# Kernel optimization log

Measured on AMD Instinct MI355X. Metric: run time of the kernel, lower is better.

## Reference

```python
import jax, jax.numpy as jnp
import numpy as np

N_NODES = 50000
N_EDGES = 300000
HIDDEN = 256


def setup_inputs() -> dict:
    key = jax.random.key(0)
    k_e, k_ei, k_rev, k_w, k_b = jax.random.split(key, 5)
    E = jax.random.normal(k_e, (N_EDGES, HIDDEN), dtype=jnp.float32)
    edge_index = jax.random.randint(k_ei, (2, N_EDGES), 0, N_NODES, dtype=jnp.int64)
    rev_index = jax.random.randint(k_rev, (N_EDGES,), 0, N_EDGES, dtype=jnp.int64)
    # Linear(hidden, hidden) params, torch-style: y = x @ W.T + b
    W = jax.random.normal(k_w, (HIDDEN, HIDDEN), dtype=jnp.float32) * (1.0 / np.sqrt(HIDDEN))
    b = jax.random.normal(k_b, (HIDDEN,), dtype=jnp.float32) * 0.01
    return {"E": E, "edge_index": edge_index, "rev_index": rev_index, "W": W, "b": b}


def reference(E, edge_index, rev_index, W, b):
    src, dest = edge_index[0], edge_index[1]
    H_uv = jax.nn.relu(E)                                   # [n_edges, hidden]
    # scatter-reduce (sum) edge messages into destination nodes
    M_v = jax.ops.segment_sum(H_uv, dest, num_segments=N_NODES)  # [n_nodes, hidden]
    # gather back to edges, subtract reverse-edge message
    M_uv = M_v[src] - H_uv[rev_index]                       # [n_edges, hidden]
    # linear update (dropout p=0 is identity)
    return M_uv @ W.T + b                                   # [n_edges, hidden]
```

## Files before the change

kernel.cpp:

```cpp
#include <hip/hip_runtime.h>
#include <hip/hip_bf16.h>

typedef unsigned short ushort_t;
typedef __attribute__((ext_vector_type(8))) short short8;
typedef __attribute__((ext_vector_type(4))) float f32x4;

#define HIDDEN 256
#define N_NODES 50000
#define BM 64
#define LDSROW 512

__device__ __forceinline__ unsigned int f2bf(float f) {
    union { float f; unsigned int i; } v; v.f = f;
    return (v.i + 0x7fffu + ((v.i >> 16) & 1u)) >> 16;
}
__device__ __forceinline__ float bf2f(unsigned int u) {
    union { unsigned int i; float f; } v; v.i = u << 16; return v.f;
}

#define OFF_MVB    0u
#define OFF_WF     25600000u
#define OFF_CNT    25731072u
#define OFF_OFFS   25931072u
#define OFF_CUR    26131076u
#define OFF_ELIST  26331076u
#define OFF_BSUM   27531076u

#define SCAN_NBLK ((N_NODES + 255) / 256)

__global__ void convert_w_frag(const float* __restrict__ W, ushort_t* __restrict__ Wf, int n) {
    int i = blockIdx.x * blockDim.x + threadIdx.x;
    if (i >= n) return;
    const int t    = i & 7;
    const int lane = (i >> 3) & 63;
    const int kk   = (i >> 9) & 7;
    const int g    = i >> 12;
    const int j = g * 16 + (lane & 15);
    const int k = kk * 32 + ((lane >> 4) & 3) * 8 + t;
    Wf[i] = (ushort_t)f2bf(W[j * HIDDEN + k]);
}

__global__ void count_dst(const int* __restrict__ dst, int* __restrict__ cnt, int n) {
    int i = blockIdx.x * blockDim.x + threadIdx.x;
    if (i < n) atomicAdd(&cnt[dst[i]], 1);
}

__global__ __launch_bounds__(256)
void block_scan(const int* __restrict__ cnt, int* __restrict__ offs,
                int* __restrict__ bsum) {
    __shared__ int sh[256];
    const int t = threadIdx.x;
    const int idx = blockIdx.x * 256 + t;
    int v = (idx < N_NODES) ? cnt[idx] : 0;
    sh[t] = v;
    __syncthreads();
    for (int off = 1; off < 256; off <<= 1) {
        int x = (t >= off) ? sh[t - off] : 0;
        __syncthreads();
        sh[t] += x;
        __syncthreads();
    }
    if (idx < N_NODES) offs[idx] = sh[t] - v;
    if (t == 255) bsum[blockIdx.x] = sh[255];
}

__global__ __launch_bounds__(256)
void scan_bsum(int* __restrict__ bsum, int nb) {
    __shared__ int sh[256];
    const int t = threadIdx.x;
    int v = (t < nb) ? bsum[t] : 0;
    sh[t] = v;
    __syncthreads();
    for (int off = 1; off < 256; off <<= 1) {
        int x = (t >= off) ? sh[t - off] : 0;
        __syncthreads();
        sh[t] += x;
        __syncthreads();
    }
    if (t < nb) bsum[t] = sh[t] - v;
}

__global__ __launch_bounds__(256)
void add_base(int* __restrict__ offs, const int* __restrict__ bsum,
              int* __restrict__ cur, int n_edges) {
    const int idx = blockIdx.x * 256 + threadIdx.x;
    if (idx < N_NODES) {
        int o = offs[idx] + bsum[idx >> 8];
        offs[idx] = o;
        cur[idx] = o;
    }
    if (idx == 0) offs[N_NODES] = n_edges;
}

__global__ void fill_elist(const int* __restrict__ dst, int* __restrict__ cur,
                           int* __restrict__ elist, int n) {
    int i = blockIdx.x * blockDim.x + threadIdx.x;
    if (i < n) {
        int d = dst[i];
        int pos = atomicAdd(&cur[d], 1);
        elist[pos] = i;
    }
}

__global__ __launch_bounds__(256)
void node_gather_sum(const float* __restrict__ E,
                     const int* __restrict__ offs,
                     const int* __restrict__ elist,
                     unsigned int* __restrict__ Mvb) {
    const int w    = blockIdx.x * 4 + (threadIdx.x >> 6);
    const int node = w >> 1;
    const int half = w & 1;
    const int lane = threadIdx.x & 63;
    if (node >= N_NODES) return;
    const float* Eh = E + half * 128 + lane * 2;
    const int s0 = offs[node];
    const int s1 = offs[node + 1];
    float ax = 0.f, ay = 0.f;
    int j = s0;
    for (; j + 4 <= s1; j += 4) {
        const int e0 = elist[j], e1 = elist[j + 1], e2 = elist[j + 2], e3 = elist[j + 3];
        float2 v0 = *(const float2*)(Eh + (size_t)e0 * HIDDEN);
        float2 v1 = *(const float2*)(Eh + (size_t)e1 * HIDDEN);
        float2 v2 = *(const float2*)(Eh + (size_t)e2 * HIDDEN);
        float2 v3 = *(const float2*)(Eh + (size_t)e3 * HIDDEN);
        ax += fmaxf(v0.x, 0.f) + fmaxf(v1.x, 0.f) + fmaxf(v2.x, 0.f) + fmaxf(v3.x, 0.f);
        ay += fmaxf(v0.y, 0.f) + fmaxf(v1.y, 0.f) + fmaxf(v2.y, 0.f) + fmaxf(v3.y, 0.f);
    }
    for (; j < s1; ++j) {
        float2 v = *(const float2*)(Eh + (size_t)elist[j] * HIDDEN);
        ax += fmaxf(v.x, 0.f);
        ay += fmaxf(v.y, 0.f);
    }
    Mvb[(size_t)node * 128 + half * 64 + lane] = f2bf(ax) | (f2bf(ay) << 16);
}

__global__ __launch_bounds__(256, 3)
void gemm_fused(const float* __restrict__ E,
                const int* __restrict__ src,
                const int* __restrict__ rev,
                const unsigned int* __restrict__ Mvb,
                const ushort_t* __restrict__ Wf,
                const float* __restrict__ bias,
                float* __restrict__ out, int n_edges) {
    __shared__ __align__(16) unsigned char lds[BM * LDSROW];
    const int tid = threadIdx.x;
    const int row0 = blockIdx.x * BM;
    const int lane = tid & 63;
    const int wid  = tid >> 6;

    {
        const int wrow = wid * 16;
#pragma unroll
        for (int rr = 0; rr < 16; rr += 4) {
            float4 ev[4];
            uint2  mv[4];
            const int rbase = wrow + rr;
#pragma unroll
            for (int i = 0; i < 4; ++i) {
                int gr = row0 + rbase + i;
                int grc = (gr < n_edges) ? gr : (n_edges - 1);
                const int s  = src[grc];
                const int rv = rev[grc];
                ev[i] = *(const float4*)(E + (size_t)rv * HIDDEN + lane * 4);
                mv[i] = *(const uint2*)(Mvb + (size_t)s * (HIDDEN / 2) + lane * 2);
            }
#pragma unroll
            for (int i = 0; i < 4; ++i) {
                const int r = rbase + i;
                uint2 o;
                o.x = f2bf(bf2f(mv[i].x & 0xffffu) - fmaxf(ev[i].x, 0.f)) |
                      (f2bf(bf2f(mv[i].x >> 16)    - fmaxf(ev[i].y, 0.f)) << 16);
                o.y = f2bf(bf2f(mv[i].y & 0xffffu) - fmaxf(ev[i].z, 0.f)) |
                      (f2bf(bf2f(mv[i].y >> 16)    - fmaxf(ev[i].w, 0.f)) << 16);
                const int slot = (lane >> 1) ^ (r & 7);
                *(uint2*)(lds + r * LDSROW + slot * 16 + (lane & 1) * 8) = o;
            }
        }
    }
    __syncthreads();

    const int l15   = lane & 15;
    const int hi16  = lane >> 4;
    const int wcol0 = wid * 64;
    const int r7l   = l15 & 7;

    f32x4 acc[4][4];
#pragma unroll
    for (int m = 0; m < 4; ++m)
#pragma unroll
        for (int n = 0; n < 4; ++n)
            acc[m][n] = (f32x4){0.f, 0.f, 0.f, 0.f};

#pragma unroll 2
    for (int kk = 0; kk < 8; ++kk) {
        const int slotbyte = ((kk * 4 + hi16) ^ r7l) * 16;
        short8 a[4], bfr[4];
#pragma unroll
        for (int m = 0; m < 4; ++m)
            a[m] = *(const short8*)(lds + (m * 16 + l15) * LDSROW + slotbyte);
#pragma unroll
        for (int n = 0; n < 4; ++n)
            bfr[n] = *(const short8*)(Wf + (size_t)((((wid * 4 + n) * 8 + kk) * 64 + lane) << 3));
#pragma unroll
        for (int m = 0; m < 4; ++m)
#pragma unroll
            for (int n = 0; n < 4; ++n)
                acc[m][n] = __builtin_amdgcn_mfma_f32_16x16x32_bf16(bfr[n], a[m], acc[m][n], 0, 0, 0);
    }

#pragma unroll
    for (int m = 0; m < 4; ++m) {
        const int row = row0 + m * 16 + l15;
        if (row < n_edges) {
            float* orow = out + (size_t)row * HIDDEN;
#pragma unroll
            for (int n = 0; n < 4; ++n) {
                const int cb = wcol0 + n * 16 + hi16 * 4;
                float4 bv = *(const float4*)(bias + cb);
                float4 o;
                o.x = acc[m][n][0] + bv.x;
                o.y = acc[m][n][1] + bv.y;
                o.z = acc[m][n][2] + bv.z;
                o.w = acc[m][n][3] + bv.w;
                *(float4*)(orow + cb) = o;
            }
        }
    }
}

extern "C" void kernel_launch(void* const* d_in, const int* in_sizes, int n_in,
                              void* d_out, int out_size, void* d_ws, size_t ws_size,
                              hipStream_t stream) {
    const float* E    = (const float*)d_in[0];
    const int*   ei   = (const int*)d_in[1];
    const int*   rev  = (const int*)d_in[2];
    const float* W    = (const float*)d_in[3];
    const float* bias = (const float*)d_in[4];
    float* out = (float*)d_out;
    const int n_edges = in_sizes[2];
    const int* srcI = ei;
    const int* dstI = ei + n_edges;

    char* ws = (char*)d_ws;
    unsigned int* Mvb  = (unsigned int*)(ws + OFF_MVB);
    ushort_t*     Wf   = (ushort_t*)(ws + OFF_WF);
    int*          cnt  = (int*)(ws + OFF_CNT);
    int*          offs = (int*)(ws + OFF_OFFS);
    int*          cur  = (int*)(ws + OFF_CUR);
    int*          elst = (int*)(ws + OFF_ELIST);
    int*          bsum = (int*)(ws + OFF_BSUM);

    hipMemsetAsync(cnt, 0, N_NODES * sizeof(int), stream);

    convert_w_frag<<<(HIDDEN * HIDDEN + 255) / 256, 256, 0, stream>>>(W, Wf, HIDDEN * HIDDEN);

    count_dst<<<(n_edges + 255) / 256, 256, 0, stream>>>(dstI, cnt, n_edges);
    block_scan<<<SCAN_NBLK, 256, 0, stream>>>(cnt, offs, bsum);
    scan_bsum<<<1, 256, 0, stream>>>(bsum, SCAN_NBLK);
    add_base<<<SCAN_NBLK, 256, 0, stream>>>(offs, bsum, cur, n_edges);
    fill_elist<<<(n_edges + 255) / 256, 256, 0, stream>>>(dstI, cur, elst, n_edges);

    const int nwaves = N_NODES * 2;
    node_gather_sum<<<(nwaves + 3) / 4, 256, 0, stream>>>(E, offs, elst, Mvb);

    const int nblk = (n_edges + BM - 1) / BM;
    gemm_fused<<<nblk, 256, 0, stream>>>(E, srcI, rev, Mvb, Wf, bias, out, n_edges);
}
```

Before: 286.1 us.

## Make GEMM wave-independent with 16-row tiles per wave, drop block barrier

The fused gather+GEMM kernel is restructured so each wave owns a 16-row tile and computes all 256 output columns, staging its rows in a private LDS slice. This removes the block-wide __syncthreads and raises the occupancy hint from 3 to 4. In exchange, W fragments are now loaded by every wave for all 16 column groups instead of each wave loading a quarter, so global/L2 traffic for W rises. The hipMemsetAsync is also replaced with a small zeroing kernel.

After: 339.3 us. 18.6% more time.

```diff
diff --git a/kernel.cpp b/kernel.cpp
--- a/kernel.cpp
+++ b/kernel.cpp
@@ -7,8 +7,6 @@
 
 #define HIDDEN 256
 #define N_NODES 50000
-#define BM 64
-#define LDSROW 512
 
 __device__ __forceinline__ unsigned int f2bf(float f) {
     union { float f; unsigned int i; } v; v.f = f;
@@ -38,6 +36,11 @@
     const int j = g * 16 + (lane & 15);
     const int k = kk * 32 + ((lane >> 4) & 3) * 8 + t;
     Wf[i] = (ushort_t)f2bf(W[j * HIDDEN + k]);
+}
+
+__global__ void zero_i32(int* __restrict__ p, int n) {
+    int i = blockIdx.x * blockDim.x + threadIdx.x;
+    if (i < n) p[i] = 0;
 }
 
 __global__ void count_dst(const int* __restrict__ dst, int* __restrict__ cnt, int n) {
@@ -134,96 +137,78 @@
     Mvb[(size_t)node * 128 + half * 64 + lane] = f2bf(ax) | (f2bf(ay) << 16);
 }
 
-__global__ __launch_bounds__(256, 3)
-void gemm_fused(const float* __restrict__ E,
-                const int* __restrict__ src,
-                const int* __restrict__ rev,
-                const unsigned int* __restrict__ Mvb,
-                const ushort_t* __restrict__ Wf,
-                const float* __restrict__ bias,
-                float* __restrict__ out, int n_edges) {
-    __shared__ __align__(16) unsigned char lds[BM * LDSROW];
-    const int tid = threadIdx.x;
-    const int row0 = blockIdx.x * BM;
+__global__ __launch_bounds__(256, 4)
+void gemm_wave(const float* __restrict__ E,
+               const int* __restrict__ src,
+               const int* __restrict__ rev,
+               const unsigned int* __restrict__ Mvb,
+               const ushort_t* __restrict__ Wf,
+               const float* __restrict__ bias,
+               float* __restrict__ out, int n_edges) {
+    __shared__ __align__(16) unsigned char lds[4 * 16 * 512];
+    const int tid  = threadIdx.x;
     const int lane = tid & 63;
     const int wid  = tid >> 6;
-
-    {
-        const int wrow = wid * 16;
-#pragma unroll
-        for (int rr = 0; rr < 16; rr += 4) {
-            float4 ev[4];
-            uint2  mv[4];
-            const int rbase = wrow + rr;
-#pragma unroll
-            for (int i = 0; i < 4; ++i) {
-                int gr = row0 + rbase + i;
-                int grc = (gr < n_edges) ? gr : (n_edges - 1);
-                const int s  = src[grc];
-                const int rv = rev[grc];
-                ev[i] = *(const float4*)(E + (size_t)rv * HIDDEN + lane * 4);
-                mv[i] = *(const uint2*)(Mvb + (size_t)s * (HIDDEN / 2) + lane * 2);
-            }
-#pragma unroll
-            for (int i = 0; i < 4; ++i) {
-                const int r = rbase + i;
-                uint2 o;
-                o.x = f2bf(bf2f(mv[i].x & 0xffffu) - fmaxf(ev[i].x, 0.f)) |
-                      (f2bf(bf2f(mv[i].x >> 16)    - fmaxf(ev[i].y, 0.f)) << 16);
-                o.y = f2bf(bf2f(mv[i].y & 0xffffu) - fmaxf(ev[i].z, 0.f)) |
-                      (f2bf(bf2f(mv[i].y >> 16)    - fmaxf(ev[i].w, 0.f)) << 16);
-                const int slot = (lane >> 1) ^ (r & 7);
-                *(uint2*)(lds + r * LDSROW + slot * 16 + (lane & 1) * 8) = o;
-            }
-        }
-    }
-    __syncthreads();
-
-    const int l15   = lane & 15;
-    const int hi16  = lane >> 4;
-    const int wcol0 = wid * 64;
-    const int r7l   = l15 & 7;
-
-    f32x4 acc[4][4];
-#pragma unroll
-    for (int m = 0; m < 4; ++m)
-#pragma unroll
-        for (int n = 0; n < 4; ++n)
-            acc[m][n] = (f32x4){0.f, 0.f, 0.f, 0.f};
-
-#pragma unroll 2
+    const int l15  = lane & 15;
+    const int hi16 = lane >> 4;
+    const int row0 = (blockIdx.x * 4 + wid) * 16;
+    if (row0 >= n_edges) return;
+    unsigned char* mylds = lds + wid * 8192;
+
+#pragma unroll
+    for (int b = 0; b < 2; ++b) {
+        float4 ev[8];
+        uint2  mv[8];
+#pragma unroll
+        for (int i = 0; i < 8; ++i) {
+            int gr = row0 + b * 8 + i;
+            int grc = (gr < n_edges) ? gr : (n_edges - 1);
+            ev[i] = *(const float4*)(E + (size_t)rev[grc] * HIDDEN + lane * 4);
+            mv[i] = *(const uint2*)(Mvb + (size_t)src[grc] * 128 + lane * 2);
+        }
+#pragma unroll
+        for (int i = 0; i < 8; ++i) {
+            const int r = b * 8 + i;
+            uint2 o;
+            o.x = f2bf(bf2f(mv[i].x & 0xffffu) - fmaxf(ev[i].x, 0.f)) |
+                  (f2bf(bf2f(mv[i].x >> 16)    - fmaxf(ev[i].y, 0.f)) << 16);
+            o.y = f2bf(bf2f(mv[i].y & 0xffffu) - fmaxf(ev[i].z, 0.f)) |
+                  (f2bf(bf2f(mv[i].y >> 16)    - fmaxf(ev[i].w, 0.f)) << 16);
+            const int slot = (lane >> 1) ^ (r & 7);
+            *(uint2*)(mylds + r * 512 + slot * 16 + (lane & 1) * 8) = o;
+        }
+    }
+
+    f32x4 acc[16];
+#pragma unroll
+    for (int n = 0; n < 16; ++n)
+        acc[n] = (f32x4){0.f, 0.f, 0.f, 0.f};
+
+    const int r7l = l15 & 7;
+#pragma unroll 1
     for (int kk = 0; kk < 8; ++kk) {
         const int slotbyte = ((kk * 4 + hi16) ^ r7l) * 16;
-        short8 a[4], bfr[4];
-#pragma unroll
-        for (int m = 0; m < 4; ++m)
-            a[m] = *(const short8*)(lds + (m * 16 + l15) * LDSROW + slotbyte);
-#pragma unroll
-        for (int n = 0; n < 4; ++n)
-            bfr[n] = *(const short8*)(Wf + (size_t)((((wid * 4 + n) * 8 + kk) * 64 + lane) << 3));
-#pragma unroll
-        for (int m = 0; m < 4; ++m)
-#pragma unroll
-            for (int n = 0; n < 4; ++n)
-                acc[m][n] = __builtin_amdgcn_mfma_f32_16x16x32_bf16(bfr[n], a[m], acc[m][n], 0, 0, 0);
-    }
-
-#pragma unroll
-    for (int m = 0; m < 4; ++m) {
-        const int row = row0 + m * 16 + l15;
-        if (row < n_edges) {
-            float* orow = out + (size_t)row * HIDDEN;
-#pragma unroll
-            for (int n = 0; n < 4; ++n) {
-                const int cb = wcol0 + n * 16 + hi16 * 4;
-                float4 bv = *(const float4*)(bias + cb);
-                float4 o;
-                o.x = acc[m][n][0] + bv.x;
-                o.y = acc[m][n][1] + bv.y;
-                o.z = acc[m][n][2] + bv.z;
-                o.w = acc[m][n][3] + bv.w;
-                *(float4*)(orow + cb) = o;
-            }
+        short8 a = *(const short8*)(mylds + l15 * 512 + slotbyte);
+#pragma unroll
+        for (int n = 0; n < 16; ++n) {
+            short8 bfr = *(const short8*)(Wf + (size_t)(((n * 8 + kk) * 64 + lane) << 3));
+            acc[n] = __builtin_amdgcn_mfma_f32_16x16x32_bf16(bfr, a, acc[n], 0, 0, 0);
+        }
+    }
+
+    const int row = row0 + l15;
+    if (row < n_edges) {
+        float* orow = out + (size_t)row * HIDDEN;
+#pragma unroll
+        for (int n = 0; n < 16; ++n) {
+            const int cb = n * 16 + hi16 * 4;
+            float4 bv = *(const float4*)(bias + cb);
+            float4 o;
+            o.x = acc[n][0] + bv.x;
+            o.y = acc[n][1] + bv.y;
+            o.z = acc[n][2] + bv.z;
+            o.w = acc[n][3] + bv.w;
+            *(float4*)(orow + cb) = o;
         }
     }
 }
@@ -250,8 +235,7 @@
     int*          elst = (int*)(ws + OFF_ELIST);
     int*          bsum = (int*)(ws + OFF_BSUM);
 
-    hipMemsetAsync(cnt, 0, N_NODES * sizeof(int), stream);
-
+    zero_i32<<<SCAN_NBLK, 256, 0, stream>>>(cnt, N_NODES);
     convert_w_frag<<<(HIDDEN * HIDDEN + 255) / 256, 256, 0, stream>>>(W, Wf, HIDDEN * HIDDEN);
 
     count_dst<<<(n_edges + 255) / 256, 256, 0, stream>>>(dstI, cnt, n_edges);
@@ -263,6 +247,7 @@
     const int nwaves = N_NODES * 2;
     node_gather_sum<<<(nwaves + 3) / 4, 256, 0, stream>>>(E, offs, elst, Mvb);
 
-    const int nblk = (n_edges + BM - 1) / BM;
-    gemm_fused<<<nblk, 256, 0, stream>>>(E, srcI, rev, Mvb, Wf, bias, out, n_edges);
-}
+    const int ntiles = (n_edges + 15) / 16;
+    const int nblk = (ntiles + 3) / 4;
+    gemm_wave<<<nblk, 256, 0, stream>>>(E, srcI, rev, Mvb, Wf, bias, out, n_edges);
+}
```

## Apply linear layer per edge first, then aggregate projected messages

Applied to the files above, without the earlier changes.

Uses linearity to compute P = relu(E) @ W.T per edge once with a streaming (non-gathered) GEMM, stored as bf16. Node sums of P are then gathered into Q, and an elementwise emit kernel computes Q[src] - P[rev] + b. The memset is also folded into the weight-prep kernel. The trade is an extra bf16 intermediate of edge size plus an fp32 node buffer, and rounding P to bf16 before the sum, in exchange for removing the random gathers from the GEMM's load phase.

After: 330.0 us. 1.15x slower.

```diff
diff --git a/kernel.cpp b/kernel.cpp
--- a/kernel.cpp
+++ b/kernel.cpp
@@ -8,7 +8,6 @@
 #define HIDDEN 256
 #define N_NODES 50000
 #define BM 64
-#define LDSROW 512
 
 __device__ __forceinline__ unsigned int f2bf(float f) {
     union { float f; unsigned int i; } v; v.f = f;
@@ -18,26 +17,30 @@
     union { unsigned int i; float f; } v; v.i = u << 16; return v.f;
 }
 
-#define OFF_MVB    0u
-#define OFF_WF     25600000u
-#define OFF_CNT    25731072u
-#define OFF_OFFS   25931072u
-#define OFF_CUR    26131076u
-#define OFF_ELIST  26331076u
-#define OFF_BSUM   27531076u
+#define OFF_P      0u
+#define OFF_Q      153600000u
+#define OFF_WF     204800000u
+#define OFF_CNT    204931072u
+#define OFF_OFFS   205131072u
+#define OFF_CUR    205331076u
+#define OFF_ELIST  205531076u
+#define OFF_BSUM   206731076u
 
 #define SCAN_NBLK ((N_NODES + 255) / 256)
 
-__global__ void convert_w_frag(const float* __restrict__ W, ushort_t* __restrict__ Wf, int n) {
+__global__ void prep(const float* __restrict__ W, ushort_t* __restrict__ Wf,
+                     int* __restrict__ cnt) {
     int i = blockIdx.x * blockDim.x + threadIdx.x;
-    if (i >= n) return;
-    const int t    = i & 7;
-    const int lane = (i >> 3) & 63;
-    const int kk   = (i >> 9) & 7;
-    const int g    = i >> 12;
-    const int j = g * 16 + (lane & 15);
-    const int k = kk * 32 + ((lane >> 4) & 3) * 8 + t;
-    Wf[i] = (ushort_t)f2bf(W[j * HIDDEN + k]);
+    if (i < N_NODES) cnt[i] = 0;
+    if (i < HIDDEN * HIDDEN) {
+        const int t    = i & 7;
+        const int lane = (i >> 3) & 63;
+        const int kk   = (i >> 9) & 7;
+        const int g    = i >> 12;
+        const int j = g * 16 + (lane & 15);
+        const int k = kk * 32 + ((lane >> 4) & 3) * 8 + t;
+        Wf[i] = (ushort_t)f2bf(W[j * HIDDEN + k]);
+    }
 }
 
 __global__ void count_dst(const int* __restrict__ dst, int* __restrict__ cnt, int n) {
@@ -102,47 +105,11 @@
     }
 }
 
-__global__ __launch_bounds__(256)
-void node_gather_sum(const float* __restrict__ E,
-                     const int* __restrict__ offs,
-                     const int* __restrict__ elist,
-                     unsigned int* __restrict__ Mvb) {
-    const int w    = blockIdx.x * 4 + (threadIdx.x >> 6);
-    const int node = w >> 1;
-    const int half = w & 1;
-    const int lane = threadIdx.x & 63;
-    if (node >= N_NODES) return;
-    const float* Eh = E + half * 128 + lane * 2;
-    const int s0 = offs[node];
-    const int s1 = offs[node + 1];
-    float ax = 0.f, ay = 0.f;
-    int j = s0;
-    for (; j + 4 <= s1; j += 4) {
-        const int e0 = elist[j], e1 = elist[j + 1], e2 = elist[j + 2], e3 = elist[j + 3];
-        float2 v0 = *(const float2*)(Eh + (size_t)e0 * HIDDEN);
-        float2 v1 = *(const float2*)(Eh + (size_t)e1 * HIDDEN);
-        float2 v2 = *(const float2*)(Eh + (size_t)e2 * HIDDEN);
-        float2 v3 = *(const float2*)(Eh + (size_t)e3 * HIDDEN);
-        ax += fmaxf(v0.x, 0.f) + fmaxf(v1.x, 0.f) + fmaxf(v2.x, 0.f) + fmaxf(v3.x, 0.f);
-        ay += fmaxf(v0.y, 0.f) + fmaxf(v1.y, 0.f) + fmaxf(v2.y, 0.f) + fmaxf(v3.y, 0.f);
-    }
-    for (; j < s1; ++j) {
-        float2 v = *(const float2*)(Eh + (size_t)elist[j] * HIDDEN);
-        ax += fmaxf(v.x, 0.f);
-        ay += fmaxf(v.y, 0.f);
-    }
-    Mvb[(size_t)node * 128 + half * 64 + lane] = f2bf(ax) | (f2bf(ay) << 16);
-}
-
 __global__ __launch_bounds__(256, 3)
-void gemm_fused(const float* __restrict__ E,
-                const int* __restrict__ src,
-                const int* __restrict__ rev,
-                const unsigned int* __restrict__ Mvb,
-                const ushort_t* __restrict__ Wf,
-                const float* __restrict__ bias,
-                float* __restrict__ out, int n_edges) {
-    __shared__ __align__(16) unsigned char lds[BM * LDSROW];
+void gemm_P(const float* __restrict__ E,
+            const ushort_t* __restrict__ Wf,
+            unsigned int* __restrict__ P, int n_edges) {
+    __shared__ __align__(16) unsigned char lds[BM * 512];
     const int tid = threadIdx.x;
     const int row0 = blockIdx.x * BM;
     const int lane = tid & 63;
@@ -151,29 +118,22 @@
     {
         const int wrow = wid * 16;
 #pragma unroll
-        for (int rr = 0; rr < 16; rr += 4) {
-            float4 ev[4];
-            uint2  mv[4];
-            const int rbase = wrow + rr;
-#pragma unroll
-            for (int i = 0; i < 4; ++i) {
-                int gr = row0 + rbase + i;
+        for (int b = 0; b < 2; ++b) {
+            float4 ev[8];
+#pragma unroll
+            for (int i = 0; i < 8; ++i) {
+                int gr = row0 + wrow + b * 8 + i;
                 int grc = (gr < n_edges) ? gr : (n_edges - 1);
-                const int s  = src[grc];
-                const int rv = rev[grc];
-                ev[i] = *(const float4*)(E + (size_t)rv * HIDDEN + lane * 4);
-                mv[i] = *(const uint2*)(Mvb + (size_t)s * (HIDDEN / 2) + lane * 2);
+                ev[i] = *(const float4*)(E + (size_t)grc * HIDDEN + lane * 4);
             }
 #pragma unroll
-            for (int i = 0; i < 4; ++i) {
-                const int r = rbase + i;
+            for (int i = 0; i < 8; ++i) {
+                const int r = wrow + b * 8 + i;
                 uint2 o;
-                o.x = f2bf(bf2f(mv[i].x & 0xffffu) - fmaxf(ev[i].x, 0.f)) |
-                      (f2bf(bf2f(mv[i].x >> 16)    - fmaxf(ev[i].y, 0.f)) << 16);
-                o.y = f2bf(bf2f(mv[i].y & 0xffffu) - fmaxf(ev[i].z, 0.f)) |
-                      (f2bf(bf2f(mv[i].y >> 16)    - fmaxf(ev[i].w, 0.f)) << 16);
+                o.x = f2bf(fmaxf(ev[i].x, 0.f)) | (f2bf(fmaxf(ev[i].y, 0.f)) << 16);
+                o.y = f2bf(fmaxf(ev[i].z, 0.f)) | (f2bf(fmaxf(ev[i].w, 0.f)) << 16);
                 const int slot = (lane >> 1) ^ (r & 7);
-                *(uint2*)(lds + r * LDSROW + slot * 16 + (lane & 1) * 8) = o;
+                *(uint2*)(lds + r * 512 + slot * 16 + (lane & 1) * 8) = o;
             }
         }
     }
@@ -197,7 +157,7 @@
         short8 a[4], bfr[4];
 #pragma unroll
         for (int m = 0; m < 4; ++m)
-            a[m] = *(const short8*)(lds + (m * 16 + l15) * LDSROW + slotbyte);
+            a[m] = *(const short8*)(lds + (m * 16 + l15) * 512 + slotbyte);
 #pragma unroll
         for (int n = 0; n < 4; ++n)
             bfr[n] = *(const short8*)(Wf + (size_t)((((wid * 4 + n) * 8 + kk) * 64 + lane) << 3));
@@ -212,18 +172,84 @@
     for (int m = 0; m < 4; ++m) {
         const int row = row0 + m * 16 + l15;
         if (row < n_edges) {
-            float* orow = out + (size_t)row * HIDDEN;
+            unsigned int* prow = P + (size_t)row * (HIDDEN / 2);
 #pragma unroll
             for (int n = 0; n < 4; ++n) {
                 const int cb = wcol0 + n * 16 + hi16 * 4;
-                float4 bv = *(const float4*)(bias + cb);
-                float4 o;
-                o.x = acc[m][n][0] + bv.x;
-                o.y = acc[m][n][1] + bv.y;
-                o.z = acc[m][n][2] + bv.z;
-                o.w = acc[m][n][3] + bv.w;
-                *(float4*)(orow + cb) = o;
+                uint2 o;
+                o.x = f2bf(acc[m][n][0]) | (f2bf(acc[m][n][1]) << 16);
+                o.y = f2bf(acc[m][n][2]) | (f2bf(acc[m][n][3]) << 16);
+                *(uint2*)(prow + (cb >> 1)) = o;
             }
+        }
+    }
+}
+
+__global__ __launch_bounds__(256)
+void q_gather(const unsigned int* __restrict__ P,
+              const int* __restrict__ offs,
+              const int* __restrict__ elist,
+              float* __restrict__ Q) {
+    const int node = blockIdx.x * 4 + (threadIdx.x >> 6);
+    const int lane = threadIdx.x & 63;
+    if (node >= N_NODES) return;
+    const int d0 = offs[node];
+    const int d1 = offs[node + 1];
+    float q0 = 0.f, q1 = 0.f, q2 = 0.f, q3 = 0.f;
+    int j = d0;
+    for (; j + 4 <= d1; j += 4) {
+        const int e0 = elist[j], e1 = elist[j + 1], e2 = elist[j + 2], e3 = elist[j + 3];
+        uint2 p0 = *(const uint2*)(P + (size_t)e0 * 128 + lane * 2);
+        uint2 p1 = *(const uint2*)(P + (size_t)e1 * 128 + lane * 2);
+        uint2 p2 = *(const uint2*)(P + (size_t)e2 * 128 + lane * 2);
+        uint2 p3 = *(const uint2*)(P + (size_t)e3 * 128 + lane * 2);
+        q0 += bf2f(p0.x & 0xffffu) + bf2f(p1.x & 0xffffu) + bf2f(p2.x & 0xffffu) + bf2f(p3.x & 0xffffu);
+        q1 += bf2f(p0.x >> 16)     + bf2f(p1.x >> 16)     + bf2f(p2.x >> 16)     + bf2f(p3.x >> 16);
+        q2 += bf2f(p0.y & 0xffffu) + bf2f(p1.y & 0xffffu) + bf2f(p2.y & 0xffffu) + bf2f(p3.y & 0xffffu);
+        q3 += bf2f(p0.y >> 16)     + bf2f(p1.y >> 16)     + bf2f(p2.y >> 16)     + bf2f(p3.y >> 16);
+    }
+    for (; j < d1; ++j) {
+        uint2 p = *(const uint2*)(P + (size_t)elist[j] * 128 + lane * 2);
+        q0 += bf2f(p.x & 0xffffu);
+        q1 += bf2f(p.x >> 16);
+        q2 += bf2f(p.y & 0xffffu);
+        q3 += bf2f(p.y >> 16);
+    }
+    float4 o = {q0, q1, q2, q3};
+    *(float4*)(Q + (size_t)node * HIDDEN + lane * 4) = o;
+}
+
+__global__ __launch_bounds__(256)
+void emit(const float* __restrict__ Q,
+          const unsigned int* __restrict__ P,
+          const int* __restrict__ src,
+          const int* __restrict__ rev,
+          const float* __restrict__ bias,
+          float* __restrict__ out, int n_edges) {
+    const int wave = blockIdx.x * 4 + (threadIdx.x >> 6);
+    const int lane = threadIdx.x & 63;
+    const int e0 = wave * 4;
+    if (e0 >= n_edges) return;
+    const int nr = (n_edges - e0 < 4) ? (n_edges - e0) : 4;
+
+    float4 qv[4];
+    uint2  pv[4];
+#pragma unroll
+    for (int i = 0; i < 4; ++i) {
+        int e = e0 + ((i < nr) ? i : 0);
+        qv[i] = *(const float4*)(Q + (size_t)src[e] * HIDDEN + lane * 4);
+        pv[i] = *(const uint2*)(P + (size_t)rev[e] * 128 + lane * 2);
+    }
+    float4 bv = *(const float4*)(bias + lane * 4);
+#pragma unroll
+    for (int i = 0; i < 4; ++i) {
+        if (i < nr) {
+            float4 o;
+            o.x = qv[i].x - bf2f(pv[i].x & 0xffffu) + bv.x;
+            o.y = qv[i].y - bf2f(pv[i].x >> 16)     + bv.y;
+            o.z = qv[i].z - bf2f(pv[i].y & 0xffffu) + bv.z;
+            o.w = qv[i].w - bf2f(pv[i].y >> 16)     + bv.w;
+            *(float4*)(out + (size_t)(e0 + i) * HIDDEN + lane * 4) = o;
         }
     }
 }
@@ -242,7 +268,8 @@
     const int* dstI = ei + n_edges;
 
     char* ws = (char*)d_ws;
-    unsigned int* Mvb  = (unsigned int*)(ws + OFF_MVB);
+    unsigned int* P    = (unsigned int*)(ws + OFF_P);
+    float*        Q    = (float*)(ws + OFF_Q);
     ushort_t*     Wf   = (ushort_t*)(ws + OFF_WF);
     int*          cnt  = (int*)(ws + OFF_CNT);
     int*          offs = (int*)(ws + OFF_OFFS);
@@ -250,9 +277,7 @@
     int*          elst = (int*)(ws + OFF_ELIST);
     int*          bsum = (int*)(ws + OFF_BSUM);
 
-    hipMemsetAsync(cnt, 0, N_NODES * sizeof(int), stream);
-
-    convert_w_frag<<<(HIDDEN * HIDDEN + 255) / 256, 256, 0, stream>>>(W, Wf, HIDDEN * HIDDEN);
+    prep<<<(HIDDEN * HIDDEN + 255) / 256, 256, 0, stream>>>(W, Wf, cnt);
 
     count_dst<<<(n_edges + 255) / 256, 256, 0, stream>>>(dstI, cnt, n_edges);
     block_scan<<<SCAN_NBLK, 256, 0, stream>>>(cnt, offs, bsum);
@@ -260,9 +285,11 @@
     add_base<<<SCAN_NBLK, 256, 0, stream>>>(offs, bsum, cur, n_edges);
     fill_elist<<<(n_edges + 255) / 256, 256, 0, stream>>>(dstI, cur, elst, n_edges);
 
-    const int nwaves = N_NODES * 2;
-    node_gather_sum<<<(nwaves + 3) / 4, 256, 0, stream>>>(E, offs, elst, Mvb);
-
     const int nblk = (n_edges + BM - 1) / BM;
-    gemm_fused<<<nblk, 256, 0, stream>>>(E, srcI, rev, Mvb, Wf, bias, out, n_edges);
-}
+    gemm_P<<<nblk, 256, 0, stream>>>(E, Wf, P, n_edges);
+
+    q_gather<<<(N_NODES + 3) / 4, 256, 0, stream>>>(P, offs, elst, Q);
+
+    const int nwave = (n_edges + 3) / 4;
+    emit<<<(nwave + 3) / 4, 256, 0, stream>>>(Q, P, srcI, rev, bias, out, n_edges);
+}
```
